# Kernel tuning notes

Hardware: AMD Instinct MI355X
Metric: run time of the kernel (lower is better)

Reference implementation:

```python
import jax, jax.numpy as jnp
import numpy as np

EPS = 1e-5
TOP_K = 2


def setup_inputs() -> dict:
    key = jax.random.key(0)
    ks = jax.random.split(key, 8)
    B, T, D, E, F = 4, 2048, 1024, 8, 4096
    s_in = 1.0 / np.sqrt(D)
    s_ff = 1.0 / np.sqrt(F)
    return {
        "hidden_states": jax.random.normal(ks[0], (B, T, D), jnp.float32),
        "input_tensor": jax.random.normal(ks[1], (B, T, D), jnp.float32),
        "gate_w": jax.random.normal(ks[2], (D, E), jnp.float32) * s_in,
        "gate_b": jnp.zeros((E,), jnp.float32),
        "w1": jax.random.normal(ks[3], (E, D, F), jnp.float32) * s_in,
        "b1": jnp.zeros((E, F), jnp.float32),
        "w2": jax.random.normal(ks[4], (E, F, D), jnp.float32) * s_ff,
        "b2": jnp.zeros((E, D), jnp.float32),
        "gamma": jnp.ones((D,), jnp.float32),
        "beta": jnp.zeros((D,), jnp.float32),
    }


def _layer_norm(x, gamma, beta):
    mu = jnp.mean(x, axis=-1, keepdims=True)
    var = jnp.mean(jnp.square(x - mu), axis=-1, keepdims=True)
    return (x - mu) * jax.lax.rsqrt(var + EPS) * gamma + beta


def reference(hidden_states, input_tensor, gate_w, gate_b, w1, b1, w2, b2, gamma, beta):
    E = gate_b.shape[0]
    # Router: softmax over experts, then top-k gate values/indices.
    gate_logits = jnp.einsum("btd,de->bte", hidden_states, gate_w) + gate_b
    gate_probs = jax.nn.softmax(gate_logits, axis=-1)
    topk_gates, topk_idx = jax.lax.top_k(gate_probs, TOP_K)  # [B,T,K]
    # Combine weights per expert: sum of top-k gate values routed to expert e.
    combine_w = jnp.sum(
        jax.nn.one_hot(topk_idx, E, dtype=hidden_states.dtype)
        * topk_gates[..., None],
        axis=-2,
    )  # [B,T,E]
    # Dispatch/combine: weighted sum of expert FFN outputs (loop over small fixed E).
    expert_outputs = jnp.zeros_like(hidden_states)
    for e in range(E):
        h = jax.nn.gelu(jnp.einsum("btd,df->btf", hidden_states, w1[e]) + b1[e])
        y = jnp.einsum("btf,fd->btd", h, w2[e]) + b2[e]
        expert_outputs = expert_outputs + combine_w[..., e:e + 1] * y
    # Dropout is identity in eval mode.
    return _layer_norm(expert_outputs + input_tensor, gamma, beta)
```

## Files before the change

kernel.cpp:

```cpp
#include <hip/hip_runtime.h>

#define TOKENS 8192
#define DIM 1024
#define NEXP 8
#define FDIM 4096

typedef __bf16 bf16x8 __attribute__((ext_vector_type(8)));
typedef float f32x4 __attribute__((ext_vector_type(4)));
typedef float f32x16 __attribute__((ext_vector_type(16)));

__device__ __forceinline__ unsigned short f2bf(float f) {
  unsigned u = __builtin_bit_cast(unsigned, f);
  u += 0x7fffu + ((u >> 16) & 1u);
  return (unsigned short)(u >> 16);
}

__device__ __forceinline__ float bf2f(unsigned short s) {
  unsigned u = (unsigned)s << 16;
  return __builtin_bit_cast(float, u);
}

__device__ __forceinline__ void gload16(const void* g, void* l) {
  __builtin_amdgcn_global_load_lds(
      (const __attribute__((address_space(1))) unsigned int*)g,
      (__attribute__((address_space(3))) unsigned int*)l, 16, 0, 0);
}

__global__ void prep_kernel(const float* __restrict__ w1,
                            unsigned short* __restrict__ w1t,
                            const float* __restrict__ w2,
                            unsigned short* __restrict__ w2t,
                            const float* __restrict__ hs,
                            const float* __restrict__ gw,
                            const float* __restrict__ gb,
                            int* __restrict__ counts,
                            int* __restrict__ tok_idx,
                            float* __restrict__ tok_w,
                            unsigned int* __restrict__ slotinfo,
                            unsigned short* __restrict__ hs_bf) {
  __shared__ unsigned int lt[64][64];
  const int L = blockIdx.x;

  if (L < 2048) {
    const int lane = threadIdx.x & 63;
    const int wid = threadIdx.x >> 6;
    const int t = L * 4 + wid;
    const float* row = hs + (size_t)t * DIM;

    float x[16];
    const float4* r4 = (const float4*)(row + lane * 16);
#pragma unroll
    for (int i = 0; i < 4; ++i) {
      float4 v = r4[i];
      x[i * 4 + 0] = v.x; x[i * 4 + 1] = v.y; x[i * 4 + 2] = v.z; x[i * 4 + 3] = v.w;
    }

    float acc[8];
#pragma unroll
    for (int e = 0; e < 8; ++e) acc[e] = 0.f;
#pragma unroll
    for (int i = 0; i < 16; ++i) {
      const int d = lane * 16 + i;
      const float4* g4 = (const float4*)(gw + (size_t)d * 8);
      float4 g0 = g4[0], g1 = g4[1];
      const float xv = x[i];
      acc[0] += xv * g0.x; acc[1] += xv * g0.y; acc[2] += xv * g0.z; acc[3] += xv * g0.w;
      acc[4] += xv * g1.x; acc[5] += xv * g1.y; acc[6] += xv * g1.z; acc[7] += xv * g1.w;
    }
#pragma unroll
    for (int sh = 1; sh < 64; sh <<= 1) {
#pragma unroll
      for (int e = 0; e < 8; ++e) acc[e] += __shfl_xor(acc[e], sh, 64);
    }
#pragma unroll
    for (int e = 0; e < 8; ++e) acc[e] += gb[e];

    float mx = acc[0];
#pragma unroll
    for (int e = 1; e < 8; ++e) mx = fmaxf(mx, acc[e]);
    float p[8];
    float sum = 0.f;
#pragma unroll
    for (int e = 0; e < 8; ++e) { p[e] = __expf(acc[e] - mx); sum += p[e]; }
    const float inv = 1.0f / sum;

    int i0 = 0; float b0 = p[0];
#pragma unroll
    for (int e = 1; e < 8; ++e) if (p[e] > b0) { b0 = p[e]; i0 = e; }
    int i1 = -1; float b1v = -1.f;
#pragma unroll
    for (int e = 0; e < 8; ++e) if (e != i0 && p[e] > b1v) { b1v = p[e]; i1 = e; }

    if (lane == 0) {
      int pos0 = atomicAdd(&counts[i0], 1);
      tok_idx[i0 * TOKENS + pos0] = t;
      tok_w[i0 * TOKENS + pos0] = b0 * inv;
      int pos1 = atomicAdd(&counts[i1], 1);
      tok_idx[i1 * TOKENS + pos1] = t;
      tok_w[i1 * TOKENS + pos1] = b1v * inv;
      slotinfo[t] = ((unsigned)i0 << 29) | ((unsigned)pos0 << 16) |
                    ((unsigned)i1 << 13) | (unsigned)pos1;
    }

    unsigned short us[16];
#pragma unroll
    for (int i = 0; i < 16; ++i) us[i] = f2bf(x[i]);
    uint4 o0, o1;
    o0.x = (unsigned)us[0] | ((unsigned)us[1] << 16);
    o0.y = (unsigned)us[2] | ((unsigned)us[3] << 16);
    o0.z = (unsigned)us[4] | ((unsigned)us[5] << 16);
    o0.w = (unsigned)us[6] | ((unsigned)us[7] << 16);
    o1.x = (unsigned)us[8] | ((unsigned)us[9] << 16);
    o1.y = (unsigned)us[10] | ((unsigned)us[11] << 16);
    o1.z = (unsigned)us[12] | ((unsigned)us[13] << 16);
    o1.w = (unsigned)us[14] | ((unsigned)us[15] << 16);
    uint4* dst = (uint4*)(hs_bf + (size_t)t * DIM + lane * 16);
    dst[0] = o0;
    dst[1] = o1;
    return;
  }

  const int bi = L - 2048;
  const float* src;
  unsigned short* dstp;
  int R, C, bi2;
  if (bi < 4096) { src = w1; dstp = w1t; R = DIM;  C = FDIM; bi2 = bi; }
  else           { src = w2; dstp = w2t; R = FDIM; C = DIM;  bi2 = bi - 4096; }
  const int e = bi2 >> 9;
  const int w = bi2 & 511;
  const int nft = C >> 6;
  const int dt = w / nft, ft = w % nft;
  const int r0 = dt * 128, c0 = ft * 64;
  const float* s = src + (size_t)e * R * C;
  unsigned short* dout = dstp + (size_t)e * R * C;
  const int tid = threadIdx.x;

#pragma unroll
  for (int pi = 0; pi < 4; ++pi) {
    const int idx = tid + pi * 256;
    const int dp = idx >> 4;
    const int f0 = (idx & 15) * 4;
    const float4 va = *(const float4*)(s + (size_t)(r0 + dp * 2) * C + c0 + f0);
    const float4 vb = *(const float4*)(s + (size_t)(r0 + dp * 2 + 1) * C + c0 + f0);
    const float a[4] = {va.x, va.y, va.z, va.w};
    const float b[4] = {vb.x, vb.y, vb.z, vb.w};
#pragma unroll
    for (int j = 0; j < 4; ++j) {
      const int f = f0 + j;
      lt[f][dp ^ (((f >> 2) & 7) << 2)] =
          (unsigned)f2bf(a[j]) | ((unsigned)f2bf(b[j]) << 16);
    }
  }
  __syncthreads();
#pragma unroll
  for (int wi = 0; wi < 4; ++wi) {
    const int idx = tid + wi * 256;
    const int f = idx >> 4;
    const int dp0 = (idx & 15) * 4;
    const int sw = ((f >> 2) & 7) << 2;
    uint4 o = *(const uint4*)&lt[f][dp0 ^ sw];
    *(uint4*)(dout + (size_t)(c0 + f) * R + r0 + dp0 * 2) = o;
  }
}

template<int MODE, int K, int N>
__global__ __launch_bounds__(256, 4)
void moe_gemm(const unsigned short* __restrict__ Abase,
              const unsigned short* __restrict__ Bbase,
              const float* __restrict__ bias,
              const int* __restrict__ counts,
              const int* __restrict__ tok_idx,
              unsigned short* __restrict__ dst) {
  constexpr int NS = K / 32;
  constexpr int NQ = (MODE == 0) ? 8 : 2;
  __shared__ __align__(16) unsigned char sm[32768];

  const int L = blockIdx.x;
  const int xk = L & 7;
  const int tt = L >> 3;
  const int g = (tt >> 4) * 8 + xk;
  const int within = tt & 15;

  int e = 0, mcq = 0, n4 = 0, goff = 0, cnt = 0;
  {
    int accC = 0, accOff = 0;
    bool found = false;
#pragma unroll
    for (int ee = 0; ee < NEXP; ++ee) {
      const int c = counts[ee];
      const int mt = (c + 127) >> 7;
      const int mc4 = (mt + 3) >> 2;
      const int ch = mc4 * NQ;
      if (!found && g < accC + ch) {
        const int local = g - accC;
        e = ee;
        mcq = (local / NQ) * 4;
        n4 = (local % NQ) * 4;
        goff = accOff;
        cnt = c;
        found = true;
      }
      accC += ch;
      accOff += c;
    }
    if (!found) return;
  }
  const int m0 = (mcq + (within >> 2)) * 128;
  if (m0 >= cnt) return;
  const int n0 = (n4 + (within & 3)) * 128;

  const int tid = threadIdx.x;
  const int lane = tid & 63;
  const int wid = tid >> 6;
  const int wm = wid >> 1;
  const int wn = wid & 1;
  const int l31 = lane & 31;
  const int lh = lane >> 5;

  const int trow = tid >> 2;
  const int tswz = (tid & 3) ^ ((trow >> 1) & 3) ^ ((trow >> 3) & 3);
  const unsigned char* Bexp = (const unsigned char*)(Bbase + (size_t)e * K * N);

  int gA0 = m0 + trow;      if (gA0 > cnt - 1) gA0 = cnt - 1;
  int gA1 = m0 + trow + 64; if (gA1 > cnt - 1) gA1 = cnt - 1;
  size_t rowA0, rowA1;
  if (MODE == 0) {
    rowA0 = (size_t)tok_idx[e * TOKENS + gA0] * K;
    rowA1 = (size_t)tok_idx[e * TOKENS + gA1] * K;
  } else {
    rowA0 = (size_t)(goff + gA0) * K;
    rowA1 = (size_t)(goff + gA1) * K;
  }
  const unsigned char* pA0 = (const unsigned char*)(Abase + rowA0) + tswz * 16;
  const unsigned char* pA1 = (const unsigned char*)(Abase + rowA1) + tswz * 16;
  const unsigned char* pB0 = Bexp + (size_t)(n0 + trow) * (K * 2) + tswz * 16;
  const unsigned char* pB1 = Bexp + (size_t)(n0 + trow + 64) * (K * 2) + tswz * 16;

  const int sw = ((l31 >> 1) & 3) ^ ((l31 >> 3) & 3);
  const int cE = lh ^ sw;
  const int aB = wm * 4096 + l31 * 64 + cE * 16;
  const int bB = 8192 + wn * 4096 + l31 * 64 + cE * 16;
  const unsigned char* smc = (const unsigned char*)sm;
  unsigned char* smw = (unsigned char*)sm + tid * 16;

  f32x16 acc[2][2];
#pragma unroll
  for (int mb = 0; mb < 2; ++mb)
#pragma unroll
    for (int nb = 0; nb < 2; ++nb)
#pragma unroll
      for (int r = 0; r < 16; ++r) acc[mb][nb][r] = 0.f;

  gload16(pA0, smw);
  gload16(pA1, smw + 4096);
  gload16(pB0, smw + 8192);
  gload16(pB1, smw + 12288);
  pA0 += 64; pA1 += 64; pB0 += 64; pB1 += 64;

#pragma unroll 1
  for (int st = 0; st < NS; ++st) {
    const int cs = (st & 1) << 14;
    const int ns = ((st + 1) & 1) << 14;
    if (st < NS - 1) {
      gload16(pA0, smw + ns);
      gload16(pA1, smw + ns + 4096);
      gload16(pB0, smw + ns + 8192);
      gload16(pB1, smw + ns + 12288);
      pA0 += 64; pA1 += 64; pB0 += 64; pB1 += 64;
      asm volatile("s_waitcnt vmcnt(4)" ::: "memory");
    } else {
      asm volatile("s_waitcnt vmcnt(0)" ::: "memory");
    }
    __builtin_amdgcn_s_barrier();
    __builtin_amdgcn_sched_barrier(0);
#pragma unroll
    for (int kq = 0; kq < 2; ++kq) {
      const int ko = kq << 5;
      bf16x8 a0 = *(const bf16x8*)(smc + cs + (aB ^ ko));
      bf16x8 a1 = *(const bf16x8*)(smc + cs + ((aB + 2048) ^ ko));
      bf16x8 b0 = *(const bf16x8*)(smc + cs + (bB ^ ko));
      bf16x8 b1 = *(const bf16x8*)(smc + cs + ((bB + 2048) ^ ko));
      acc[0][0] = __builtin_amdgcn_mfma_f32_32x32x16_bf16(a0, b0, acc[0][0], 0, 0, 0);
      acc[0][1] = __builtin_amdgcn_mfma_f32_32x32x16_bf16(a0, b1, acc[0][1], 0, 0, 0);
      acc[1][0] = __builtin_amdgcn_mfma_f32_32x32x16_bf16(a1, b0, acc[1][0], 0, 0, 0);
      acc[1][1] = __builtin_amdgcn_mfma_f32_32x32x16_bf16(a1, b1, acc[1][1], 0, 0, 0);
    }
    __builtin_amdgcn_sched_barrier(0);
    asm volatile("s_waitcnt lgkmcnt(0)" ::: "memory");
    __builtin_amdgcn_s_barrier();
  }

#pragma unroll
  for (int nb = 0; nb < 2; ++nb) {
    const int fcol = n0 + wn * 64 + nb * 32 + l31;
    const float bv = bias[e * N + fcol];
#pragma unroll
    for (int mb = 0; mb < 2; ++mb) {
#pragma unroll
      for (int r = 0; r < 16; ++r) {
        const int ml = wm * 64 + mb * 32 + (r & 3) + 8 * (r >> 2) + 4 * lh;
        const int gm = m0 + ml;
        if (gm < cnt) {
          float v = acc[mb][nb][r] + bv;
          if (MODE == 0) {
            const float u = 0.7978845608028654f * (v + 0.044715f * v * v * v);
            const float th = 1.0f - 2.0f / (1.0f + __expf(2.0f * u));
            v = 0.5f * v * (1.0f + th);
          }
          dst[(size_t)(goff + gm) * N + fcol] = f2bf(v);
        }
      }
    }
  }
}

__global__ void ln_combine_kernel(const unsigned short* __restrict__ y_buf,
                                  const float* __restrict__ in_t,
                                  const int* __restrict__ counts,
                                  const unsigned int* __restrict__ slotinfo,
                                  const float* __restrict__ tok_w,
                                  const float* __restrict__ gamma,
                                  const float* __restrict__ beta,
                                  float* __restrict__ out) {
  const int lane = threadIdx.x & 63;
  const int wid = threadIdx.x >> 6;
  const int t = blockIdx.x * 4 + wid;

  const unsigned s = slotinfo[t];
  const int e0 = s >> 29, p0 = (s >> 16) & 8191;
  const int e1 = (s >> 13) & 7, p1 = s & 8191;
  int off0 = 0, off1 = 0;
#pragma unroll
  for (int ee = 0; ee < NEXP; ++ee) {
    const int c = counts[ee];
    if (ee < e0) off0 += c;
    if (ee < e1) off1 += c;
  }
  const float w0 = tok_w[e0 * TOKENS + p0];
  const float w1 = tok_w[e1 * TOKENS + p1];
  const size_t r0 = (size_t)(off0 + p0) * DIM;
  const size_t r1 = (size_t)(off1 + p1) * DIM;

  float v[16];
  {
    const float4* i4 = (const float4*)(in_t + (size_t)t * DIM + lane * 16);
    const uint4* y0 = (const uint4*)(y_buf + r0 + lane * 16);
    const uint4* y1 = (const uint4*)(y_buf + r1 + lane * 16);
#pragma unroll
    for (int i = 0; i < 4; ++i) {
      float4 a = i4[i];
      v[i * 4 + 0] = a.x; v[i * 4 + 1] = a.y; v[i * 4 + 2] = a.z; v[i * 4 + 3] = a.w;
    }
#pragma unroll
    for (int i = 0; i < 2; ++i) {
      uint4 u0 = y0[i];
      uint4 u1 = y1[i];
      const unsigned uw0[4] = {u0.x, u0.y, u0.z, u0.w};
      const unsigned uw1[4] = {u1.x, u1.y, u1.z, u1.w};
#pragma unroll
      for (int k = 0; k < 4; ++k) {
        const int base = i * 8 + k * 2;
        v[base + 0] += w0 * bf2f((unsigned short)(uw0[k] & 0xffff)) +
                       w1 * bf2f((unsigned short)(uw1[k] & 0xffff));
        v[base + 1] += w0 * bf2f((unsigned short)(uw0[k] >> 16)) +
                       w1 * bf2f((unsigned short)(uw1[k] >> 16));
      }
    }
  }

  float sum = 0.f, s2 = 0.f;
#pragma unroll
  for (int i = 0; i < 16; ++i) { sum += v[i]; s2 += v[i] * v[i]; }
#pragma unroll
  for (int sh = 1; sh < 64; sh <<= 1) {
    sum += __shfl_xor(sum, sh, 64);
    s2 += __shfl_xor(s2, sh, 64);
  }
  const float mu = sum * (1.0f / DIM);
  const float var = s2 * (1.0f / DIM) - mu * mu;
  const float rs = rsqrtf(var + 1e-5f);

  float4* w4 = (float4*)(out + (size_t)t * DIM + lane * 16);
#pragma unroll
  for (int i = 0; i < 4; ++i) {
    const int d = lane * 16 + i * 4;
    float4 gg = *(const float4*)(gamma + d);
    float4 bb = *(const float4*)(beta + d);
    float4 o;
    o.x = (v[i * 4 + 0] - mu) * rs * gg.x + bb.x;
    o.y = (v[i * 4 + 1] - mu) * rs * gg.y + bb.y;
    o.z = (v[i * 4 + 2] - mu) * rs * gg.z + bb.z;
    o.w = (v[i * 4 + 3] - mu) * rs * gg.w + bb.w;
    w4[i] = o;
  }
}

extern "C" void kernel_launch(void* const* d_in, const int* in_sizes, int n_in,
                              void* d_out, int out_size, void* d_ws, size_t ws_size,
                              hipStream_t stream) {
  const float* hs    = (const float*)d_in[0];
  const float* in_t  = (const float*)d_in[1];
  const float* gw    = (const float*)d_in[2];
  const float* gb    = (const float*)d_in[3];
  const float* w1    = (const float*)d_in[4];
  const float* b1    = (const float*)d_in[5];
  const float* w2    = (const float*)d_in[6];
  const float* b2    = (const float*)d_in[7];
  const float* gamma = (const float*)d_in[8];
  const float* beta  = (const float*)d_in[9];
  float* out = (float*)d_out;
  char* ws = (char*)d_ws;

  int* counts            = (int*)(ws + 0);
  unsigned int* slotinfo = (unsigned int*)(ws + 512);
  int* tok_idx           = (int*)(ws + 66048);
  float* tok_w           = (float*)(ws + 328192);
  unsigned short* hs_bf  = (unsigned short*)(ws + 590336);
  unsigned short* w1t    = (unsigned short*)(ws + 17367552);
  unsigned short* w2t    = (unsigned short*)(ws + 84476416);
  unsigned short* h_buf  = (unsigned short*)(ws + 151585280);
  unsigned short* y_buf  = (unsigned short*)(ws + 590336);

  hipMemsetAsync(counts, 0, NEXP * sizeof(int), stream);
  prep_kernel<<<10240, 256, 0, stream>>>(w1, w1t, w2, w2t,
                                         hs, gw, gb, counts, tok_idx, tok_w,
                                         slotinfo, hs_bf);
  moe_gemm<0, DIM, FDIM><<<6144, 256, 0, stream>>>(
      hs_bf, w1t, b1, counts, tok_idx, h_buf);
  moe_gemm<1, FDIM, DIM><<<2048, 256, 0, stream>>>(
      h_buf, w2t, b2, counts, tok_idx, y_buf);
  ln_combine_kernel<<<TOKENS / 4, 256, 0, stream>>>(y_buf, in_t, counts, slotinfo,
                                                    tok_w, gamma, beta, out);
}
```

Before: 711.5 us.

## Overlap w2 transpose/convert with first expert GEMM by interleaving blocks

Moves the fp32-to-bf16 transpose of w2 out of the prep kernel and into the first expert GEMM launch. Every five blocks of that launch, two do a w2 transpose tile and three do GEMM work, so the memory-bound conversion can overlap with compute-bound MFMA work. This shortens the prep kernel but adds blocks and a branch to the GEMM kernel. Those extra blocks may compete for occupancy and cache.

Measured after the change: 709.5 us. About the same (-0.3%).

```diff
diff --git a/kernel.cpp b/kernel.cpp
--- a/kernel.cpp
+++ b/kernel.cpp
@@ -26,10 +26,49 @@
       (__attribute__((address_space(3))) unsigned int*)l, 16, 0, 0);
 }
 
+__device__ __forceinline__ void transpose_tile(const float* __restrict__ src,
+                                               unsigned short* __restrict__ dstp,
+                                               int R, int C, int bi2,
+                                               void* smraw, int tid) {
+  unsigned int (*lt)[64] = (unsigned int(*)[64])smraw;
+  const int e = bi2 >> 9;
+  const int w = bi2 & 511;
+  const int nft = C >> 6;
+  const int dt = w / nft, ft = w % nft;
+  const int r0 = dt * 128, c0 = ft * 64;
+  const float* s = src + (size_t)e * R * C;
+  unsigned short* dout = dstp + (size_t)e * R * C;
+
+#pragma unroll
+  for (int pi = 0; pi < 4; ++pi) {
+    const int idx = tid + pi * 256;
+    const int dp = idx >> 4;
+    const int f0 = (idx & 15) * 4;
+    const float4 va = *(const float4*)(s + (size_t)(r0 + dp * 2) * C + c0 + f0);
+    const float4 vb = *(const float4*)(s + (size_t)(r0 + dp * 2 + 1) * C + c0 + f0);
+    const float a[4] = {va.x, va.y, va.z, va.w};
+    const float b[4] = {vb.x, vb.y, vb.z, vb.w};
+#pragma unroll
+    for (int j = 0; j < 4; ++j) {
+      const int f = f0 + j;
+      lt[f][dp ^ (((f >> 2) & 7) << 2)] =
+          (unsigned)f2bf(a[j]) | ((unsigned)f2bf(b[j]) << 16);
+    }
+  }
+  __syncthreads();
+#pragma unroll
+  for (int wi = 0; wi < 4; ++wi) {
+    const int idx = tid + wi * 256;
+    const int f = idx >> 4;
+    const int dp0 = (idx & 15) * 4;
+    const int sw = ((f >> 2) & 7) << 2;
+    uint4 o = *(const uint4*)&lt[f][dp0 ^ sw];
+    *(uint4*)(dout + (size_t)(c0 + f) * R + r0 + dp0 * 2) = o;
+  }
+}
+
 __global__ void prep_kernel(const float* __restrict__ w1,
                             unsigned short* __restrict__ w1t,
-                            const float* __restrict__ w2,
-                            unsigned short* __restrict__ w2t,
                             const float* __restrict__ hs,
                             const float* __restrict__ gw,
                             const float* __restrict__ gb,
@@ -120,47 +159,7 @@
     return;
   }
 
-  const int bi = L - 2048;
-  const float* src;
-  unsigned short* dstp;
-  int R, C, bi2;
-  if (bi < 4096) { src = w1; dstp = w1t; R = DIM;  C = FDIM; bi2 = bi; }
-  else           { src = w2; dstp = w2t; R = FDIM; C = DIM;  bi2 = bi - 4096; }
-  const int e = bi2 >> 9;
-  const int w = bi2 & 511;
-  const int nft = C >> 6;
-  const int dt = w / nft, ft = w % nft;
-  const int r0 = dt * 128, c0 = ft * 64;
-  const float* s = src + (size_t)e * R * C;
-  unsigned short* dout = dstp + (size_t)e * R * C;
-  const int tid = threadIdx.x;
-
-#pragma unroll
-  for (int pi = 0; pi < 4; ++pi) {
-    const int idx = tid + pi * 256;
-    const int dp = idx >> 4;
-    const int f0 = (idx & 15) * 4;
-    const float4 va = *(const float4*)(s + (size_t)(r0 + dp * 2) * C + c0 + f0);
-    const float4 vb = *(const float4*)(s + (size_t)(r0 + dp * 2 + 1) * C + c0 + f0);
-    const float a[4] = {va.x, va.y, va.z, va.w};
-    const float b[4] = {vb.x, vb.y, vb.z, vb.w};
-#pragma unroll
-    for (int j = 0; j < 4; ++j) {
-      const int f = f0 + j;
-      lt[f][dp ^ (((f >> 2) & 7) << 2)] =
-          (unsigned)f2bf(a[j]) | ((unsigned)f2bf(b[j]) << 16);
-    }
-  }
-  __syncthreads();
-#pragma unroll
-  for (int wi = 0; wi < 4; ++wi) {
-    const int idx = tid + wi * 256;
-    const int f = idx >> 4;
-    const int dp0 = (idx & 15) * 4;
-    const int sw = ((f >> 2) & 7) << 2;
-    uint4 o = *(const uint4*)&lt[f][dp0 ^ sw];
-    *(uint4*)(dout + (size_t)(c0 + f) * R + r0 + dp0 * 2) = o;
-  }
+  transpose_tile(w1, w1t, DIM, FDIM, L - 2048, lt, threadIdx.x);
 }
 
 template<int MODE, int K, int N>
@@ -170,12 +169,23 @@
               const float* __restrict__ bias,
               const int* __restrict__ counts,
               const int* __restrict__ tok_idx,
-              unsigned short* __restrict__ dst) {
+              unsigned short* __restrict__ dst,
+              const float* __restrict__ w2src,
+              unsigned short* __restrict__ w2t) {
   constexpr int NS = K / 32;
   constexpr int NQ = (MODE == 0) ? 8 : 2;
   __shared__ __align__(16) unsigned char sm[32768];
 
-  const int L = blockIdx.x;
+  int L = blockIdx.x;
+  if (MODE == 0) {
+    const int q = L / 5, r = L % 5;
+    if (r >= 3) {
+      transpose_tile(w2src, w2t, FDIM, DIM, q * 2 + (r - 3), sm, threadIdx.x);
+      return;
+    }
+    L = q * 3 + r;
+  }
+
   const int xk = L & 7;
   const int tt = L >> 3;
   const int g = (tt >> 4) * 8 + xk;
@@ -422,13 +432,12 @@
   unsigned short* y_buf  = (unsigned short*)(ws + 590336);
 
   hipMemsetAsync(counts, 0, NEXP * sizeof(int), stream);
-  prep_kernel<<<10240, 256, 0, stream>>>(w1, w1t, w2, w2t,
-                                         hs, gw, gb, counts, tok_idx, tok_w,
-                                         slotinfo, hs_bf);
-  moe_gemm<0, DIM, FDIM><<<6144, 256, 0, stream>>>(
-      hs_bf, w1t, b1, counts, tok_idx, h_buf);
+  prep_kernel<<<6144, 256, 0, stream>>>(w1, w1t, hs, gw, gb, counts, tok_idx,
+                                        tok_w, slotinfo, hs_bf);
+  moe_gemm<0, DIM, FDIM><<<10240, 256, 0, stream>>>(
+      hs_bf, w1t, b1, counts, tok_idx, h_buf, w2, w2t);
   moe_gemm<1, FDIM, DIM><<<2048, 256, 0, stream>>>(
-      h_buf, w2t, b2, counts, tok_idx, y_buf);
+      h_buf, w2t, b2, counts, tok_idx, y_buf, nullptr, nullptr);
   ln_combine_kernel<<<TOKENS / 4, 256, 0, stream>>>(y_buf, in_t, counts, slotinfo,
                                                     tok_w, gamma, beta, out);
 }
```
